# Performance work log

Measured on AMD Instinct MI355X. Metric: run time of the kernel, lower is better.

## Reference

```python
import jax, jax.numpy as jnp
import numpy as np


def _bilinear_sample(fea, x, y):
    # fea: [B,C,H,W]; x,y: [B,D,HW] pixel coords. grid_sample bilinear, zeros padding, align_corners=True
    B, C, H, W = fea.shape
    x0 = jnp.floor(x)
    y0 = jnp.floor(y)
    wx1 = x - x0
    wy1 = y - y0
    flat = fea.reshape(B, C, H * W)

    def corner(xi, yi, w):
        valid = (xi >= 0) & (xi <= W - 1) & (yi >= 0) & (yi <= H - 1)
        idx = jnp.clip(yi, 0, H - 1).astype(jnp.int32) * W + jnp.clip(xi, 0, W - 1).astype(jnp.int32)
        v = jnp.take_along_axis(flat[:, :, None, :], idx[:, None, :, :], axis=3)  # [B,C,D,HW]
        return v * (w * valid)[:, None]

    return (corner(x0, y0, (1 - wx1) * (1 - wy1)) + corner(x0 + 1, y0, wx1 * (1 - wy1))
            + corner(x0, y0 + 1, (1 - wx1) * wy1) + corner(x0 + 1, y0 + 1, wx1 * wy1))


def _build_proj(p):
    # p: [B,2,4,4] -> 4x4 with top 3x4 = K @ [R|t]
    top = jnp.einsum('bij,bjk->bik', p[:, 1, :3, :3], p[:, 0, :3, :4])
    return p[:, 0].at[:, :3, :4].set(top)


def _forward(depth_values, features, proj_matrices, depth_interval, view_weights, CostNum):
    V = features.shape[0]
    ref_fea = features[0]
    B, C, H, W = ref_fea.shape
    # inverse-depth range sampling (per-pixel, CasMVSNet-style)
    inv_d = 1.0 / depth_values[:, 0]                      # [B,H,W]
    itv = depth_interval[:, 0]                            # [B,H,W]
    low = inv_d - (CostNum / 2.0) * itv
    step = (CostNum * itv) / (CostNum - 1)                # (high-low)/(D-1)
    samp = low[:, None] + jnp.arange(CostNum, dtype=inv_d.dtype)[None, :, None, None] * step[:, None]
    depth = (1.0 / samp).reshape(B, CostNum, H * W)       # back to metric depth [B,D,HW]

    ref_inv = jnp.linalg.inv(_build_proj(proj_matrices[:, 0]))
    ys, xs = jnp.meshgrid(jnp.arange(H, dtype=inv_d.dtype), jnp.arange(W, dtype=inv_d.dtype), indexing='ij')
    xyz = jnp.stack([xs.ravel(), ys.ravel(), jnp.ones(H * W, dtype=inv_d.dtype)], 0)  # [3,HW]

    vol = jnp.zeros((B, 1, CostNum, H, W), inv_d.dtype)
    wsum = jnp.full((B, 1, 1, H, W), 1e-5, inv_d.dtype)
    for i in range(1, V):
        proj = jnp.einsum('bij,bjk->bik', _build_proj(proj_matrices[:, i]), ref_inv)
        rot_xyz = jnp.einsum('bij,jn->bin', proj[:, :3, :3], xyz)                     # [B,3,HW]
        pxyz = rot_xyz[:, :, None, :] * depth[:, None] + proj[:, :3, 3][:, :, None, None]
        gx = pxyz[:, 0] / pxyz[:, 2]
        gy = pxyz[:, 1] / pxyz[:, 2]
        warped = _bilinear_sample(features[i], gx, gy).reshape(B, C, CostNum, H, W)
        wv = (warped * ref_fea[:, :, None]).mean(axis=1, keepdims=True)               # [B,1,D,H,W]
        vw = view_weights[:, i - 1][:, None, None]                                    # [B,1,1,H,W]
        vol = vol + wv * vw
        wsum = wsum + vw
    sim = vol / wsum
    # torch broadcasts [B,1,D,H,W] into the [B,C,D,H,W] buffer -> all C channels equal
    return jnp.broadcast_to(sim, (B, C, CostNum, H, W)).reshape(B, C * CostNum, H, W)


def setup_inputs():
    key = jax.random.key(0)
    ks = jax.random.split(key, 4)
    V, B, C, H, W = 5, 2, 32, 256, 320
    features = jax.random.normal(ks[0], (V, B, C, H, W), jnp.float32)
    depth_values = jax.random.uniform(ks[1], (B, 1, H, W), jnp.float32, minval=0.5, maxval=2.0)
    depth_interval = jax.random.uniform(ks[2], (B, 1, H, W), jnp.float32, minval=0.01, maxval=0.03)
    view_weights = jax.random.uniform(ks[3], (B, V - 1, H, W), jnp.float32, minval=0.1, maxval=1.0)
    K = np.array([[300.0, 0.0, W / 2.0], [0.0, 300.0, H / 2.0], [0.0, 0.0, 1.0]], np.float32)
    proj = np.zeros((B, V, 2, 4, 4), np.float32)
    for v in range(V):
        E = np.eye(4, dtype=np.float32)
        E[0, 3] = 0.1 * v  # camera baseline along x
        proj[:, v, 0] = E
        proj[:, v, 1] = np.eye(4, dtype=np.float32)
        proj[:, v, 1, :3, :3] = K
    return {"depth_values": depth_values, "features": features, "proj_matrices": jnp.asarray(proj),
            "depth_interval": depth_interval, "depth_max": 100, "depth_min": 1, "CostNum": 4,
            "view_weights": view_weights}


def reference(depth_values, features, proj_matrices, depth_interval, depth_max, depth_min, CostNum, view_weights):
    # depth_max/depth_min are unused in the per-pixel sampling path of the original helper
    return _forward(depth_values, features, proj_matrices, depth_interval, view_weights, CostNum)
```

## Files before the change

kernel.cpp:

```cpp
#include <hip/hip_runtime.h>

static constexpr int V  = 5;
static constexpr int B  = 2;
static constexpr int C  = 32;
static constexpr int H  = 256;
static constexpr int W  = 320;
static constexpr int CN = 4;
static constexpr int HW = H * W;
static constexpr int CG = 8;
static constexpr int NG = 4;
static constexpr int XT = W / 64;
static constexpr int NBLK = XT * H * B;

static constexpr size_t PARAMS_OFF = 0;

typedef float f32x2 __attribute__((ext_vector_type(2)));
typedef float f32x4 __attribute__((ext_vector_type(4)));

__device__ __forceinline__ f32x2 ld2(const float* p) {
    f32x2 v;
    __builtin_memcpy(&v, p, sizeof(f32x2));
    return v;
}

__global__ void setup_proj_kernel(const float* __restrict__ pm, float* __restrict__ params) {
    int b = threadIdx.x;
    if (b >= B) return;

    float M[V][16];
    for (int v = 0; v < V; ++v) {
        const float* E  = pm + ((size_t)(b * V + v) * 2 + 0) * 16;
        const float* Km = pm + ((size_t)(b * V + v) * 2 + 1) * 16;
        for (int r = 0; r < 3; ++r)
            for (int c = 0; c < 4; ++c) {
                float s = 0.f;
                for (int k = 0; k < 3; ++k) s += Km[r * 4 + k] * E[k * 4 + c];
                M[v][r * 4 + c] = s;
            }
        for (int c = 0; c < 4; ++c) M[v][12 + c] = E[12 + c];
    }

    float A[9], bb[3];
    for (int r = 0; r < 3; ++r) {
        for (int c = 0; c < 3; ++c) A[r * 3 + c] = M[0][r * 4 + c];
        bb[r] = M[0][r * 4 + 3];
    }
    float det = A[0] * (A[4] * A[8] - A[5] * A[7])
              - A[1] * (A[3] * A[8] - A[5] * A[6])
              + A[2] * (A[3] * A[7] - A[4] * A[6]);
    float id = 1.f / det;
    float Ai[9];
    Ai[0] = (A[4] * A[8] - A[5] * A[7]) * id;
    Ai[1] = (A[2] * A[7] - A[1] * A[8]) * id;
    Ai[2] = (A[1] * A[5] - A[2] * A[4]) * id;
    Ai[3] = (A[5] * A[6] - A[3] * A[8]) * id;
    Ai[4] = (A[0] * A[8] - A[2] * A[6]) * id;
    Ai[5] = (A[2] * A[3] - A[0] * A[5]) * id;
    Ai[6] = (A[3] * A[7] - A[4] * A[6]) * id;
    Ai[7] = (A[1] * A[6] - A[0] * A[7]) * id;
    Ai[8] = (A[0] * A[4] - A[1] * A[3]) * id;
    float bi[3];
    for (int r = 0; r < 3; ++r)
        bi[r] = -(Ai[r * 3 + 0] * bb[0] + Ai[r * 3 + 1] * bb[1] + Ai[r * 3 + 2] * bb[2]);

    float Minv[16];
    for (int r = 0; r < 3; ++r) {
        for (int c = 0; c < 3; ++c) Minv[r * 4 + c] = Ai[r * 3 + c];
        Minv[r * 4 + 3] = bi[r];
    }
    Minv[12] = 0.f; Minv[13] = 0.f; Minv[14] = 0.f; Minv[15] = 1.f;

    for (int v = 1; v < V; ++v) {
        float* dst = params + (size_t)(b * (V - 1) + (v - 1)) * 12;
        for (int r = 0; r < 3; ++r)
            for (int c = 0; c < 4; ++c) {
                float s = 0.f;
                for (int k = 0; k < 4; ++k) s += M[v][r * 4 + k] * Minv[k * 4 + c];
                dst[r * 4 + c] = s;
            }
    }
}

__global__ __launch_bounds__(256) void fused_kernel(
    const float* __restrict__ depth_values,
    const float* __restrict__ features,
    const float* __restrict__ depth_interval,
    const float* __restrict__ view_weights,
    const float* __restrict__ params,
    float* __restrict__ out)
{
    const int tid = threadIdx.x;
    const int p   = tid & 63;
    const int g   = tid >> 6;

    const int d   = blockIdx.x;
    const int u   = d >> 3;
    const int r8  = d & 7;
    const int xt  = u % XT;
    const int rid = r8 * 64 + u / XT;
    const int y   = rid & (H - 1);
    const int b   = rid >> 8;

    const int x   = xt * 64 + p;
    const int pix = y * W + x;

    __shared__ float sp4[48];
    __shared__ float stage[NG][960];
    float* const sredp = &stage[0][0];
    float* const simp  = &stage[0][0] + 1024;

    if (tid < 48) sp4[tid] = params[(size_t)b * 48 + tid];
    __syncthreads();

    const float invd = 1.f / depth_values[(size_t)b * HW + pix];
    const float itv  = depth_interval[(size_t)b * HW + pix];
    const float low  = invd - (CN * 0.5f) * itv;
    const float step = (CN * itv) / (float)(CN - 1);
    float dep[CN];
#pragma unroll
    for (int k = 0; k < CN; ++k) dep[k] = 1.f / (low + (float)k * step);

    float vws[V - 1];
#pragma unroll
    for (int i = 0; i < V - 1; ++i)
        vws[i] = view_weights[((size_t)b * (V - 1) + i) * HW + pix];
    float wsum = 1e-5f;
#pragma unroll
    for (int i = 0; i < V - 1; ++i) wsum += vws[i];

    const float* refp = features + ((size_t)b * C + g * CG) * HW + pix;
    float rf[CG];
#pragma unroll
    for (int c = 0; c < CG; ++c) rf[c] = __builtin_nontemporal_load(refp + (size_t)c * HW);

    int soff[4];
#pragma unroll
    for (int it = 0; it < 4; ++it) {
        const int f   = (it * 64 + p) * 4;
        const int j   = (f >= 640) ? 2 : ((f >= 320) ? 1 : 0);
        const int col = f - j * 320;
        const int row = min(max(y - 1 + j, 0), H - 1);
        soff[it] = row * W + col;
    }

    const size_t VSTRIDE = (size_t)B * C * HW;
    const float* src = features + ((size_t)(B + b) * C + g * CG) * HW;

    const float fx = (float)x, fy = (float)y;
    float volsum[CN] = {0.f, 0.f, 0.f, 0.f};

    f32x4 R[4];
#pragma unroll
    for (int it = 0; it < 4; ++it)
        if (it < 3 || p < 48) R[it] = *(const f32x4*)(src + soff[it]);

    for (int iv = 0; iv < V - 1; ++iv, src += VSTRIDE) {
        const float* spv = &sp4[iv * 12];
        const float rx = spv[0] * fx + spv[1] * fy + spv[2];
        const float ry = spv[4] * fx + spv[5] * fy + spv[6];
        const float rz = spv[8] * fx + spv[9] * fy + spv[10];
        const float tx = spv[3], ty = spv[7], tz = spv[11];

        const float scale = vws[iv] * (1.f / (float)C);

        int   o0[CN];
        float wA0[CN], wB0[CN], wA1[CN], wB1[CN];
#pragma unroll
        for (int k = 0; k < CN; ++k) {
            const float dd = dep[k];
            const float px = rx * dd + tx;
            const float py = ry * dd + ty;
            const float pz = rz * dd + tz;
            const float iz = 1.f / pz;
            const float gx = px * iz;
            const float gy = py * iz;

            const float x0f = floorf(gx), y0f = floorf(gy);
            const float wx1 = gx - x0f, wy1 = gy - y0f;
            const float wx0 = 1.f - wx1, wy0 = 1.f - wy1;
            const int x0 = (int)x0f, y0 = (int)y0f;
            const int x1 = x0 + 1, y1 = y0 + 1;

            const bool vx0 = (x0 >= 0) && (x0 <= W - 1);
            const bool vx1 = (x1 >= 0) && (x1 <= W - 1);
            const bool vy0 = (y0 >= 0) && (y0 <= H - 1);
            const bool vy1 = (y1 >= 0) && (y1 <= H - 1);

            const int bx = min(max(x0, 0), W - 2);
            const int s  = x0 - bx;

            const float w00 = wx0 * wy0 * ((vx0 && vy0) ? scale : 0.f);
            const float w10 = wx1 * wy0 * ((vx1 && vy0) ? scale : 0.f);
            const float w01 = wx0 * wy1 * ((vx0 && vy1) ? scale : 0.f);
            const float w11 = wx1 * wy1 * ((vx1 && vy1) ? scale : 0.f);

            wA0[k] = (s == 0) ? w00 : ((s == -1) ? w10 : 0.f);
            wB0[k] = (s == 0) ? w10 : ((s == 1) ? w00 : 0.f);
            wA1[k] = (s == 0) ? w01 : ((s == -1) ? w11 : 0.f);
            wB1[k] = (s == 0) ? w11 : ((s == 1) ? w01 : 0.f);

            o0[k] = (y0 - y + 1) * 320 + bx;
        }

        bool okrow = true;
#pragma unroll
        for (int k = 0; k < CN; ++k)
            okrow = okrow && ((unsigned)o0[k] <= 638u);

        if (__all(okrow)) {
#pragma unroll
            for (int ch = 0; ch < CG; ++ch) {
#pragma unroll
                for (int it = 0; it < 4; ++it)
                    if (it < 3 || p < 48)
                        *(f32x4*)&stage[g][(it * 64 + p) * 4] = R[it];

                const bool more = (ch < CG - 1) || (iv < V - 2);
                if (more) {
                    const float* nsrc = (ch < CG - 1) ? src + (size_t)(ch + 1) * HW
                                                      : src + VSTRIDE;
#pragma unroll
                    for (int it = 0; it < 4; ++it)
                        if (it < 3 || p < 48) R[it] = *(const f32x4*)(nsrc + soff[it]);
                }

                const float rfc = rf[ch];
                const float* L = &stage[g][0];
#pragma unroll
                for (int k = 0; k < CN; ++k) {
                    const f32x2 a  = ld2(L + o0[k]);
                    const f32x2 b2 = ld2(L + o0[k] + 320);
                    float t = wA0[k] * a.x;
                    t = fmaf(wB0[k], a.y, t);
                    t = fmaf(wA1[k], b2.x, t);
                    t = fmaf(wB1[k], b2.y, t);
                    volsum[k] = fmaf(rfc, t, volsum[k]);
                }
            }
        } else {
#pragma unroll 1
            for (int k = 0; k < CN; ++k) {
                const float dd = dep[k];
                const float gy = (ry * dd + ty) / (rz * dd + tz);
                const int   y0 = (int)floorf(gy);
                const int  cy0 = min(max(y0,     0), H - 1);
                const int  cy1 = min(max(y0 + 1, 0), H - 1);
                const int   bx = o0[k] - (y0 - y + 1) * 320;
                const int  ib0 = cy0 * W + bx;
                const int  ib1 = cy1 * W + bx;
#pragma unroll 1
                for (int c = 0; c < CG; ++c) {
                    const float* fc  = src + (size_t)c * HW;
                    const f32x2 a   = ld2(fc + ib0);
                    const f32x2 bb2 = ld2(fc + ib1);
                    float t = wA0[k] * a.x;
                    t = fmaf(wB0[k], a.y, t);
                    t = fmaf(wA1[k], bb2.x, t);
                    t = fmaf(wB1[k], bb2.y, t);
                    volsum[k] = fmaf(rf[c], t, volsum[k]);
                }
            }
            if (iv < V - 2) {
#pragma unroll
                for (int it = 0; it < 4; ++it)
                    if (it < 3 || p < 48) R[it] = *(const f32x4*)(src + VSTRIDE + soff[it]);
            }
        }
    }

    __syncthreads();
#pragma unroll
    for (int k = 0; k < CN; ++k) sredp[(g * CN + k) * 64 + p] = volsum[k];
    __syncthreads();

    {
        const int k = g;
        const float s = sredp[(0 * CN + k) * 64 + p] + sredp[(1 * CN + k) * 64 + p]
                      + sredp[(2 * CN + k) * 64 + p] + sredp[(3 * CN + k) * 64 + p];
        simp[k * 64 + p] = s * (1.f / wsum);
    }
    __syncthreads();

    {
        const int quad = tid & 15;
        const int pc   = tid >> 4;
        float* op = out + (size_t)b * C * CN * HW + y * W + xt * 64 + quad * 4;
#pragma unroll
        for (int j = 0; j < 8; ++j) {
            const int plane = pc * 8 + j;
            const int k     = plane & 3;
            const f32x4 v   = *(const f32x4*)&simp[k * 64 + quad * 4];
            *(f32x4*)(op + (size_t)plane * HW) = v;
        }
    }
}

extern "C" void kernel_launch(void* const* d_in, const int* in_sizes, int n_in,
                              void* d_out, int out_size, void* d_ws, size_t ws_size,
                              hipStream_t stream) {
    const float* depth_values   = (const float*)d_in[0];
    const float* features       = (const float*)d_in[1];
    const float* proj_matrices  = (const float*)d_in[2];
    const float* depth_interval = (const float*)d_in[3];
    const float* view_weights   = (const float*)d_in[7];
    float* out    = (float*)d_out;
    float* params = (float*)d_ws + PARAMS_OFF;

    setup_proj_kernel<<<1, B, 0, stream>>>(proj_matrices, params);

    fused_kernel<<<NBLK, 256, 0, stream>>>(depth_values, features, depth_interval,
                                           view_weights, params, out);
}
```

Measured before the change: 288.2 us.

## Split channels between LDS staging and direct global gathers, drop cross-iteration prefetch

In the fast path, half of each group's channels are still staged into LDS rows and gathered from there, while the other half are gathered straight from global memory with precomputed row addresses. The register prefetch of the next channel or view is removed, so each channel pair loads and consumes its data within the same iteration. The aim is to halve the LDS staging traffic and register pressure and to let the global gathers overlap with the LDS work. The trade-off is more scattered, uncoalesced global loads and the loss of latency hiding across channels.

```diff
diff --git a/kernel.cpp b/kernel.cpp
--- a/kernel.cpp
+++ b/kernel.cpp
@@ -143,16 +143,15 @@
         soff[it] = row * W + col;
     }
 
+    const int rbm = max(y - 1, 0) * W;
+    const int rb0 = y * W;
+    const int rbp = min(y + 1, H - 1) * W;
+
     const size_t VSTRIDE = (size_t)B * C * HW;
     const float* src = features + ((size_t)(B + b) * C + g * CG) * HW;
 
     const float fx = (float)x, fy = (float)y;
     float volsum[CN] = {0.f, 0.f, 0.f, 0.f};
-
-    f32x4 R[4];
-#pragma unroll
-    for (int it = 0; it < 4; ++it)
-        if (it < 3 || p < 48) R[it] = *(const f32x4*)(src + soff[it]);
 
     for (int iv = 0; iv < V - 1; ++iv, src += VSTRIDE) {
         const float* spv = &sp4[iv * 12];
@@ -208,33 +207,62 @@
             okrow = okrow && ((unsigned)o0[k] <= 638u);
 
         if (__all(okrow)) {
-#pragma unroll
-            for (int ch = 0; ch < CG; ++ch) {
-#pragma unroll
-                for (int it = 0; it < 4; ++it)
-                    if (it < 3 || p < 48)
-                        *(f32x4*)&stage[g][(it * 64 + p) * 4] = R[it];
-
-                const bool more = (ch < CG - 1) || (iv < V - 2);
-                if (more) {
-                    const float* nsrc = (ch < CG - 1) ? src + (size_t)(ch + 1) * HW
-                                                      : src + VSTRIDE;
-#pragma unroll
-                    for (int it = 0; it < 4; ++it)
-                        if (it < 3 || p < 48) R[it] = *(const f32x4*)(nsrc + soff[it]);
+            int ga0[CN], ga1[CN];
+#pragma unroll
+            for (int k = 0; k < CN; ++k) {
+                const bool j1  = o0[k] >= 320;
+                const int  col = o0[k] - (j1 ? 320 : 0);
+                ga0[k] = (j1 ? rb0 : rbm) + col;
+                ga1[k] = (j1 ? rbp : rb0) + col;
+            }
+
+#pragma unroll
+            for (int q = 0; q < 4; ++q) {
+                const float* sc = src + (size_t)q * HW;
+                f32x4 Rs0, Rs1, Rs2, Rs3;
+                Rs0 = *(const f32x4*)(sc + soff[0]);
+                Rs1 = *(const f32x4*)(sc + soff[1]);
+                Rs2 = *(const f32x4*)(sc + soff[2]);
+                if (p < 48) Rs3 = *(const f32x4*)(sc + soff[3]);
+
+                const float* gc = src + (size_t)(q + 4) * HW;
+                f32x2 GA[CN], GB[CN];
+#pragma unroll
+                for (int k = 0; k < CN; ++k) {
+                    GA[k] = ld2(gc + ga0[k]);
+                    GB[k] = ld2(gc + ga1[k]);
                 }
 
-                const float rfc = rf[ch];
-                const float* L = &stage[g][0];
-#pragma unroll
-                for (int k = 0; k < CN; ++k) {
-                    const f32x2 a  = ld2(L + o0[k]);
-                    const f32x2 b2 = ld2(L + o0[k] + 320);
-                    float t = wA0[k] * a.x;
-                    t = fmaf(wB0[k], a.y, t);
-                    t = fmaf(wA1[k], b2.x, t);
-                    t = fmaf(wB1[k], b2.y, t);
-                    volsum[k] = fmaf(rfc, t, volsum[k]);
+                *(f32x4*)&stage[g][(0 * 64 + p) * 4] = Rs0;
+                *(f32x4*)&stage[g][(1 * 64 + p) * 4] = Rs1;
+                *(f32x4*)&stage[g][(2 * 64 + p) * 4] = Rs2;
+                if (p < 48) *(f32x4*)&stage[g][(3 * 64 + p) * 4] = Rs3;
+
+                {
+                    const float rfc = rf[q];
+                    const float* L = &stage[g][0];
+#pragma unroll
+                    for (int k = 0; k < CN; ++k) {
+                        const f32x2 a  = ld2(L + o0[k]);
+                        const f32x2 b2 = ld2(L + o0[k] + 320);
+                        float t = wA0[k] * a.x;
+                        t = fmaf(wB0[k], a.y, t);
+                        t = fmaf(wA1[k], b2.x, t);
+                        t = fmaf(wB1[k], b2.y, t);
+                        volsum[k] = fmaf(rfc, t, volsum[k]);
+                    }
+                }
+
+                {
+                    const float rfc = rf[q + 4];
+#pragma unroll
+                    for (int k = 0; k < CN; ++k) {
+                        float t = wA0[k] * GA[k].x;
+                        t = fmaf(wB0[k], GA[k].y, t);
+                        t = fmaf(wA1[k], GB[k].x, t);
+                        t = fmaf(wB1[k], GB[k].y, t);
+                        volsum[k] = fmaf(rfc, t, volsum[k]);
+                    }
                 }
             }
         } else {
@@ -260,11 +288,6 @@
                     volsum[k] = fmaf(rf[c], t, volsum[k]);
                 }
             }
-            if (iv < V - 2) {
-#pragma unroll
-                for (int it = 0; it < 4; ++it)
-                    if (it < 3 || p < 48) R[it] = *(const f32x4*)(src + VSTRIDE + soff[it]);
-            }
         }
     }
 
```

Result: faster. 270.4 us (-6.2%).
